# Kernel tuning notes

Measured on AMD Instinct MI355X. Metric: run time of the kernel, lower is better.

## Reference

```python
import jax, jax.numpy as jnp
import numpy as np
from jax.scipy.special import gammaln, xlogy

H, K, V = 8, 64, 192          # heads, key_size, value_size
F = 192                        # num_relative_position_features
LN2 = 0.6931471805599453


def positional_features(T):
    """Enformer positional basis: exp half-life, central mask, gamma pdf;
    non-symmetric -> concat [emb, sign(pos)*emb]. Returns [2T-1, F]."""
    n = F // 6                                  # basis per class per symmetry
    pos = jnp.arange(-(T - 1), T, dtype=jnp.float32)   # [2T-1]
    ap = jnp.abs(pos)[:, None]                  # [2T-1, 1]
    # exponential (min_half_life=3.0, seq_length=T)
    max_range = jnp.log(float(T)) / LN2
    half_life = 2.0 ** jnp.linspace(3.0, max_range, n)
    fe = jnp.exp(-LN2 / half_life * ap)
    # central mask
    widths = 2.0 ** jnp.arange(1, n + 1, dtype=jnp.float32) - 1.0
    fm = (widths > ap).astype(jnp.float32)
    # gamma (stddev=T/(2n), start_mean=T/n)
    stddev = T / (2.0 * n)
    mean = jnp.linspace(T / float(n), float(T), n)
    conc = (mean / stddev) ** 2
    rate = mean / stddev ** 2
    log_p = xlogy(conc - 1.0, ap) - rate * ap - (gammaln(conc) - conc * jnp.log(rate))
    prob = jnp.exp(log_p) + 1e-8
    fg = prob / jnp.max(prob)
    emb = jnp.concatenate([fe, fm, fg], axis=-1)               # [2T-1, F/2]
    emb = jnp.concatenate([emb, jnp.sign(pos)[:, None] * emb], axis=-1)  # [2T-1, F]
    return emb


def relative_shift(x):
    """TransformerXL relative shift. x: [B,H,T,2T-1] -> [B,H,T,T]."""
    b, h, t1, r = x.shape                       # r == 2*t1 - 1
    x = jnp.pad(x, ((0, 0), (0, 0), (0, 0), (1, 0)))  # [B,H,T,2T]
    x = x.reshape(b, h, r + 1, t1)[:, :, 1:, :]        # [B,H,2T-1,T]
    x = x.reshape(b, h, t1, r)
    return x[..., :t1]


def setup_inputs() -> dict:
    key = jax.random.key(0)
    ks = jax.random.split(key, 8)
    B, T, D = 2, 1536, 1536
    s = 0.02
    return {
        "x": jax.random.normal(ks[0], (B, T, D), jnp.float32),
        "Wq": jax.random.normal(ks[1], (D, H * K), jnp.float32) * s,
        "Wk": jax.random.normal(ks[2], (D, H * K), jnp.float32) * s,
        "Wv": jax.random.normal(ks[3], (D, H * V), jnp.float32) * s,
        "Wrk": jax.random.normal(ks[4], (F, H * K), jnp.float32) * s,
        "Wemb": jax.random.normal(ks[5], (H * V, D), jnp.float32) * s,
        "r_w_bias": jax.random.normal(ks[6], (1, H, 1, K), jnp.float32) * s,
        "r_r_bias": jax.random.normal(ks[7], (1, H, 1, K), jnp.float32) * s,
    }


def reference(x, Wq, Wk, Wv, Wrk, Wemb, r_w_bias, r_r_bias):
    B, T, D = x.shape
    q = (x @ Wq).reshape(B, T, H, K).transpose(0, 2, 1, 3)   # [B,H,T,K]
    k = (x @ Wk).reshape(B, T, H, K).transpose(0, 2, 1, 3)
    v = (x @ Wv).reshape(B, T, H, V).transpose(0, 2, 1, 3)   # [B,H,T,V]
    q = q * (K ** -0.5)                                       # scaling
    emb = positional_features(T)                              # [2T-1, F]
    r_k = (emb @ Wrk).reshape(2 * T - 1, H, K).transpose(1, 0, 2)  # [H,2T-1,K]
    content = jnp.einsum('bhqk,bhmk->bhqm', q + r_w_bias, k)       # [B,H,T,T]
    rel = jnp.einsum('bhqk,hmk->bhqm', q + r_r_bias, r_k)          # [B,H,T,2T-1]
    logits = content + relative_shift(rel)
    w = jax.nn.softmax(logits, axis=-1)
    out = jnp.einsum('bhqm,bhmv->bhqv', w, v)                      # [B,H,T,V]
    out = out.transpose(0, 2, 1, 3).reshape(B, T, H * V)
    return out @ Wemb
```

## Files before the change

### kernel.cpp

```cpp
#include <hip/hip_runtime.h>
#include <stdint.h>

#define DEVI __device__ __forceinline__

typedef short bf16x8 __attribute__((ext_vector_type(8)));
typedef float f32x4 __attribute__((ext_vector_type(4)));

#define PMAX 0.01867013f

DEVI float b2f(unsigned short u) {
  union { unsigned u32; float f; } x;
  x.u32 = ((unsigned)u) << 16;
  return x.f;
}
DEVI unsigned short f2b(float f) {
  union { float f32; unsigned u32; } x;
  x.f32 = f;
  unsigned u = x.u32;
  return (unsigned short)((u + 0x7FFFu + ((u >> 16) & 1u)) >> 16);
}

DEVI void gload16(const unsigned short* g, unsigned short* l) {
  __builtin_amdgcn_global_load_lds(
      (const __attribute__((address_space(1))) void*)g,
      (__attribute__((address_space(3))) void*)l, 16, 0, 0);
}

DEVI float gamma_prob(float ap, int i) {
  float mean = 48.f * (float)(i + 1);
  float conc = (mean / 24.f) * (mean / 24.f);
  float rate = mean / 576.f;
  if (ap == 0.f) return 1e-8f;
  float logp = (conc - 1.f) * logf(ap) - rate * ap - (lgammaf(conc) - conc * logf(rate));
  return expf(logp) + 1e-8f;
}

DEVI void dev_transpose(const float* srcf, const unsigned short* srcb, int src_ld,
                        unsigned short* dst, int dst_ld, int rows, int cols,
                        int bx, int by, unsigned short (*t)[33]) {
  int tx = threadIdx.x & 31, ty = threadIdx.x >> 5;
  int r0 = by * 32, c0 = bx * 32;
#pragma unroll
  for (int i = 0; i < 4; i++) {
    int r = r0 + ty + i * 8, cc = c0 + tx;
    if (r < rows && cc < cols)
      t[ty + i * 8][tx] = srcf ? f2b(srcf[(size_t)r * src_ld + cc])
                               : srcb[(size_t)r * src_ld + cc];
  }
  __syncthreads();
#pragma unroll
  for (int i = 0; i < 4; i++) {
    int dr = c0 + ty + i * 8, dc = r0 + tx;
    if (dr < cols && dc < rows) dst[(size_t)dr * dst_ld + dc] = t[tx][ty + i * 8];
  }
}

__global__ __launch_bounds__(256) void k_prep(
    const float* __restrict__ x, const float* __restrict__ Wq,
    const float* __restrict__ Wk, const float* __restrict__ Wv,
    const float* __restrict__ Wemb, const float* __restrict__ Wrk,
    unsigned short* __restrict__ xb, unsigned short* __restrict__ WqkvT,
    unsigned short* __restrict__ WembT, unsigned short* __restrict__ WrkT,
    unsigned short* __restrict__ emb) {
  __shared__ unsigned short t[32][33];
  int bid = blockIdx.x;
  if (bid < 4608) {
    int i = (bid * 256 + threadIdx.x) * 4;
    float4 v = *(const float4*)(x + i);
    ushort4 o;
    o.x = f2b(v.x); o.y = f2b(v.y); o.z = f2b(v.z); o.w = f2b(v.w);
    *(ushort4*)(xb + i) = o;
  } else if (bid < 5376) {
    int s = bid - 4608;
    dev_transpose(Wq, nullptr, 512, WqkvT, 1536, 1536, 512, s % 16, s / 16, t);
  } else if (bid < 6144) {
    int s = bid - 5376;
    dev_transpose(Wk, nullptr, 512, WqkvT + (size_t)512 * 1536, 1536, 1536, 512, s % 16, s / 16, t);
  } else if (bid < 8448) {
    int s = bid - 6144;
    dev_transpose(Wv, nullptr, 1536, WqkvT + (size_t)1024 * 1536, 1536, 1536, 1536, s % 48, s / 48, t);
  } else if (bid < 10752) {
    int s = bid - 8448;
    dev_transpose(Wemb, nullptr, 1536, WembT, 1536, 1536, 1536, s % 48, s / 48, t);
  } else if (bid < 10848) {
    int s = bid - 10752;
    dev_transpose(Wrk, nullptr, 512, WrkT, 192, 192, 512, s % 16, s / 16, t);
  } else {
    int idx = (bid - 10848) * 256 + threadIdx.x;
    if (idx < 3071 * 96) {
      int m = idx / 96, cc = idx % 96;
      float ap = fabsf((float)(m - 1535));
      float val;
      if (cc < 32) {
        float max_range = logf(1536.f) * 1.4426950408889634f;
        float l = 3.f + (float)cc * (max_range - 3.f) / 31.f;
        val = exp2f(-ap * exp2f(-l));
      } else if (cc < 64) {
        float width = exp2f((float)(cc - 31)) - 1.f;
        val = (width > ap) ? 1.f : 0.f;
      } else {
        val = gamma_prob(ap, cc - 64) / PMAX;
      }
      float sgn = (m > 1535) ? 1.f : ((m < 1535) ? -1.f : 0.f);
      emb[(size_t)m * 192 + cc] = f2b(val);
      emb[(size_t)m * 192 + 96 + cc] = f2b(sgn * val);
    }
  }
}

DEVI void dev_gemm(const unsigned short* __restrict__ A, const unsigned short* __restrict__ Bt,
                   unsigned short* Cb, float* Cf, int M, int N, int K,
                   int bx, int by, unsigned short* As, unsigned short* Bs) {
  int tid = threadIdx.x;
  int w = tid >> 6, L = tid & 63, g = L >> 4, c = L & 15;
  int m0 = by << 7, n0 = bx << 7;
  int wm = (w >> 1) << 6, wn = (w & 1) << 6;
  f32x4 acc[4][4];
#pragma unroll
  for (int i = 0; i < 4; i++)
#pragma unroll
    for (int j = 0; j < 4; j++) acc[i][j] = (f32x4){0.f, 0.f, 0.f, 0.f};
  int nkt = K >> 5;
  for (int kt = 0; kt < nkt; kt++) {
    int k0 = kt << 5;
#pragma unroll
    for (int i2 = 0; i2 < 2; i2++) {
      int cidx = tid + (i2 << 8);
      int row = cidx >> 2, kc = (cidx & 3) << 3;
      int ra = m0 + row;
      if (ra >= M) ra = M - 1;
      gload16(A + (size_t)ra * K + k0 + kc, As + cidx * 8);
      gload16(Bt + (size_t)(n0 + row) * K + k0 + kc, Bs + cidx * 8);
    }
    __syncthreads();
    bf16x8 af[4], bfr[4];
#pragma unroll
    for (int t = 0; t < 4; t++) af[t] = *(const bf16x8*)(As + (wm + t * 16 + c) * 32 + g * 8);
#pragma unroll
    for (int t = 0; t < 4; t++) bfr[t] = *(const bf16x8*)(Bs + (wn + t * 16 + c) * 32 + g * 8);
#pragma unroll
    for (int mt = 0; mt < 4; mt++)
#pragma unroll
      for (int nt = 0; nt < 4; nt++)
        acc[mt][nt] = __builtin_amdgcn_mfma_f32_16x16x32_bf16(af[mt], bfr[nt], acc[mt][nt], 0, 0, 0);
    __syncthreads();
  }
#pragma unroll
  for (int mt = 0; mt < 4; mt++)
#pragma unroll
    for (int nt = 0; nt < 4; nt++)
#pragma unroll
      for (int r = 0; r < 4; r++) {
        int rr = m0 + wm + mt * 16 + g * 4 + r;
        if (rr < M) {
          size_t o = (size_t)rr * N + n0 + wn + nt * 16 + c;
          if (Cf) Cf[o] = acc[mt][nt][r];
          else Cb[o] = f2b(acc[mt][nt][r]);
        }
      }
}

__global__ __launch_bounds__(256) void k_gemm(
    const unsigned short* __restrict__ A, const unsigned short* __restrict__ Bt,
    unsigned short* Cb, float* Cf, int M, int N, int K) {
  __shared__ unsigned short sm[8192];
  dev_gemm(A, Bt, Cb, Cf, M, N, K, blockIdx.x, blockIdx.y, sm, sm + 4096);
}

__global__ __launch_bounds__(256) void k_mid(
    const unsigned short* __restrict__ emb, const unsigned short* __restrict__ WrkT,
    unsigned short* __restrict__ rkb, const unsigned short* __restrict__ QKV,
    unsigned short* __restrict__ Vt) {
  __shared__ unsigned short sm[8192];
  int bid = blockIdx.x;
  if (bid < 96) {
    dev_gemm(emb, WrkT, rkb, nullptr, 3071, 512, 192, bid & 3, bid >> 2, sm, sm + 4096);
  } else {
    int tt = bid - 96;
    int which = tt / 2304;
    tt %= 2304;
    dev_transpose(nullptr, QKV + 1024 + (size_t)which * 1536 * 2560, 2560,
                  Vt + (size_t)which * 1536 * 1536, 1536, 1536, 1536,
                  tt % 48, tt / 48, (unsigned short (*)[33])sm);
  }
}

__global__ __launch_bounds__(256, 2) void k_attn(
    const unsigned short* __restrict__ QKV, const unsigned short* __restrict__ rk,
    const unsigned short* __restrict__ Vt, const float* __restrict__ rwb,
    const float* __restrict__ rrb, unsigned short* __restrict__ O) {
  __shared__ float smem[9344];
  const int tid = threadIdx.x;
  const int w = tid >> 6, L = tid & 63, g = L >> 4, c = L & 15;
  const int bid = blockIdx.x;
  const int h = bid & 7, b = (bid >> 3) & 1;
  const int i0b = (bid >> 4) << 5;
  const int bh = b * 8 + h;

  bf16x8 aqw[2][2], aqr[2][2];
#pragma unroll
  for (int qi = 0; qi < 2; qi++) {
    const unsigned short* qrow =
        QKV + (size_t)(b * 1536 + i0b + qi * 16 + c) * 2560 + h * 64;
#pragma unroll
    for (int ks = 0; ks < 2; ks++) {
      union { bf16x8 v; unsigned short s[8]; } uw, ur;
#pragma unroll
      for (int j = 0; j < 8; j++) {
        int d = ks * 32 + g * 8 + j;
        float qv = b2f(qrow[d]) * 0.125f;
        uw.s[j] = f2b(qv + rwb[h * 64 + d]);
        ur.s[j] = f2b(qv + rrb[h * 64 + d]);
      }
      aqw[qi][ks] = uw.v;
      aqr[qi][ks] = ur.v;
    }
  }

  int baddr[4], bsel[4];
#pragma unroll
  for (int r = 0; r < 4; r++) {
    int u = c - (g * 4 + r) + 15;
    baddr[r] = (((g << 4) | (u & 15)) << 2);
    bsel[r] = (u >> 4) & 1;
  }

  f32x4 Ofr[2][12];
#pragma unroll
  for (int qi = 0; qi < 2; qi++)
#pragma unroll
    for (int t = 0; t < 12; t++) Ofr[qi][t] = (f32x4){0.f, 0.f, 0.f, 0.f};
  float lrow[2][4] = {{0.f, 0.f, 0.f, 0.f}, {0.f, 0.f, 0.f, 0.f}};

  const size_t kbase = (size_t)(b * 1536) * 2560 + 512 + h * 64;
  const unsigned short* vtb = Vt + (size_t)(bh * 192) * 1536;
  const unsigned short* rkh = rk + h * 64;

  for (int jt = 0; jt < 6; jt++) {
    const int j0 = w * 384 + jt * 64;
    const int moff1 = j0 - (i0b + 16) + 1520;
    unsigned short* pwbA = (unsigned short*)smem + ((jt & 1) * 8 + w * 2 + 0) * 1152;
    unsigned short* pwbB = (unsigned short*)smem + ((jt & 1) * 8 + w * 2 + 1) * 1152;

    f32x4 Sc[2][4];
#pragma unroll
    for (int nt = 0; nt < 4; nt++) {
      const unsigned short* krow = QKV + kbase + (size_t)(j0 + nt * 16 + c) * 2560;
      bf16x8 kf0 = *(const bf16x8*)(krow + g * 8);
      bf16x8 kf1 = *(const bf16x8*)(krow + 32 + g * 8);
      f32x4 z0 = (f32x4){0.f, 0.f, 0.f, 0.f};
      z0 = __builtin_amdgcn_mfma_f32_16x16x32_bf16(aqw[0][0], kf0, z0, 0, 0, 0);
      z0 = __builtin_amdgcn_mfma_f32_16x16x32_bf16(aqw[0][1], kf1, z0, 0, 0, 0);
      Sc[0][nt] = z0;
      f32x4 z1 = (f32x4){0.f, 0.f, 0.f, 0.f};
      z1 = __builtin_amdgcn_mfma_f32_16x16x32_bf16(aqw[1][0], kf0, z1, 0, 0, 0);
      z1 = __builtin_amdgcn_mfma_f32_16x16x32_bf16(aqw[1][1], kf1, z1, 0, 0, 0);
      Sc[1][nt] = z1;
    }

    float bandp0[4], bandp1[4];
    {
      int mg = moff1 + c;
      const unsigned short* rrow = rkh + (size_t)mg * 512;
      bf16x8 rf0 = *(const bf16x8*)(rrow + g * 8);
      bf16x8 rf1 = *(const bf16x8*)(rrow + 32 + g * 8);
      f32x4 z = (f32x4){0.f, 0.f, 0.f, 0.f};
      z = __builtin_amdgcn_mfma_f32_16x16x32_bf16(aqr[1][0], rf0, z, 0, 0, 0);
      z = __builtin_amdgcn_mfma_f32_16x16x32_bf16(aqr[1][1], rf1, z, 0, 0, 0);
#pragma unroll
      for (int r = 0; r < 4; r++)
        bandp1[r] = __int_as_float(__builtin_amdgcn_ds_bpermute(baddr[r], __float_as_int(z[r])));
    }
#pragma unroll
    for (int j = 1; j <= 5; j++) {
      int mg = moff1 + 16 * j + c;
      if (mg > 3070) mg = 3070;
      const unsigned short* rrow = rkh + (size_t)mg * 512;
      bf16x8 rf0 = *(const bf16x8*)(rrow + g * 8);
      bf16x8 rf1 = *(const bf16x8*)(rrow + 32 + g * 8);
      {
        f32x4 z = (f32x4){0.f, 0.f, 0.f, 0.f};
        z = __builtin_amdgcn_mfma_f32_16x16x32_bf16(aqr[0][0], rf0, z, 0, 0, 0);
        z = __builtin_amdgcn_mfma_f32_16x16x32_bf16(aqr[0][1], rf1, z, 0, 0, 0);
        if (j == 1) {
#pragma unroll
          for (int r = 0; r < 4; r++)
            bandp0[r] = __int_as_float(__builtin_amdgcn_ds_bpermute(baddr[r], __float_as_int(z[r])));
        } else {
          const int nt = j - 2;
#pragma unroll
          for (int r = 0; r < 4; r++) {
            float bandc = __int_as_float(__builtin_amdgcn_ds_bpermute(baddr[r], __float_as_int(z[r])));
            Sc[0][nt][r] += bsel[r] ? bandc : bandp0[r];
            bandp0[r] = bandc;
          }
        }
      }
      if (j <= 4) {
        f32x4 z = (f32x4){0.f, 0.f, 0.f, 0.f};
        z = __builtin_amdgcn_mfma_f32_16x16x32_bf16(aqr[1][0], rf0, z, 0, 0, 0);
        z = __builtin_amdgcn_mfma_f32_16x16x32_bf16(aqr[1][1], rf1, z, 0, 0, 0);
        const int nt = j - 1;
#pragma unroll
        for (int r = 0; r < 4; r++) {
          float bandc = __int_as_float(__builtin_amdgcn_ds_bpermute(baddr[r], __float_as_int(z[r])));
          Sc[1][nt][r] += bsel[r] ? bandc : bandp1[r];
          bandp1[r] = bandc;
        }
      }
    }

#pragma unroll
    for (int nt = 0; nt < 4; nt++)
#pragma unroll
      for (int r = 0; r < 4; r++) {
        float pA = __expf(Sc[0][nt][r]);
        lrow[0][r] += pA;
        pwbA[(g * 4 + r) * 72 + nt * 16 + c] = f2b(pA);
        float pB = __expf(Sc[1][nt][r]);
        lrow[1][r] += pB;
        pwbB[(g * 4 + r) * 72 + nt * 16 + c] = f2b(pB);
      }
    __builtin_amdgcn_sched_barrier(0x7F);
    bf16x8 apA0 = *(const bf16x8*)(pwbA + c * 72 + g * 8);
    bf16x8 apA1 = *(const bf16x8*)(pwbA + c * 72 + 32 + g * 8);
    bf16x8 apB0 = *(const bf16x8*)(pwbB + c * 72 + g * 8);
    bf16x8 apB1 = *(const bf16x8*)(pwbB + c * 72 + 32 + g * 8);
    __builtin_amdgcn_sched_barrier(0x7F);

    __builtin_amdgcn_s_setprio(1);
#pragma unroll
    for (int nt3 = 0; nt3 < 12; nt3++) {
      const unsigned short* vrow = vtb + (size_t)(nt3 * 16 + c) * 1536 + j0;
      bf16x8 v0 = *(const bf16x8*)(vrow + g * 8);
      bf16x8 v1 = *(const bf16x8*)(vrow + 32 + g * 8);
      Ofr[0][nt3] = __builtin_amdgcn_mfma_f32_16x16x32_bf16(apA0, v0, Ofr[0][nt3], 0, 0, 0);
      Ofr[1][nt3] = __builtin_amdgcn_mfma_f32_16x16x32_bf16(apB0, v0, Ofr[1][nt3], 0, 0, 0);
      Ofr[0][nt3] = __builtin_amdgcn_mfma_f32_16x16x32_bf16(apA1, v1, Ofr[0][nt3], 0, 0, 0);
      Ofr[1][nt3] = __builtin_amdgcn_mfma_f32_16x16x32_bf16(apB1, v1, Ofr[1][nt3], 0, 0, 0);
    }
    __builtin_amdgcn_s_setprio(0);
  }

#pragma unroll
  for (int qi = 0; qi < 2; qi++)
#pragma unroll
    for (int r = 0; r < 4; r++) {
      float s = lrow[qi][r];
      s += __shfl_xor(s, 1, 64);
      s += __shfl_xor(s, 2, 64);
      s += __shfl_xor(s, 4, 64);
      s += __shfl_xor(s, 8, 64);
      lrow[qi][r] = s;
    }
  float* mll = smem + 9216;
  if (c == 0)
#pragma unroll
    for (int qi = 0; qi < 2; qi++)
#pragma unroll
      for (int r = 0; r < 4; r++) mll[qi * 64 + w * 16 + g * 4 + r] = lrow[qi][r];
  __syncthreads();
  float scale[2][4];
#pragma unroll
  for (int qi = 0; qi < 2; qi++)
#pragma unroll
    for (int r = 0; r < 4; r++) {
      int q = qi * 64 + g * 4 + r;
      scale[qi][r] = 1.f / (mll[q] + mll[16 + q] + mll[32 + q] + mll[48 + q]);
    }
#pragma unroll
  for (int qi = 0; qi < 2; qi++)
#pragma unroll
    for (int t = 0; t < 12; t++)
#pragma unroll
      for (int r = 0; r < 4; r++) Ofr[qi][t][r] *= scale[qi][r];

  const int qo = tid >> 4, v3 = (tid & 15) * 3;
#pragma unroll
  for (int qi = 0; qi < 2; qi++) {
    unsigned short* orow =
        O + (size_t)(b * 1536 + i0b + qi * 16 + qo) * 1536 + h * 192;
#pragma unroll
    for (int c4 = 0; c4 < 4; c4++) {
      __syncthreads();
      float* slot = smem + w * 768;
#pragma unroll
      for (int tl = 0; tl < 3; tl++)
#pragma unroll
        for (int r = 0; r < 4; r++)
          slot[(g * 4 + r) * 48 + tl * 16 + c] = Ofr[qi][c4 * 3 + tl][r];
      __syncthreads();
#pragma unroll
      for (int k = 0; k < 3; k++) {
        int v = v3 + k;
        float s = smem[qo * 48 + v] + smem[768 + qo * 48 + v] +
                  smem[1536 + qo * 48 + v] + smem[2304 + qo * 48 + v];
        orow[c4 * 48 + v] = f2b(s);
      }
    }
  }
}

extern "C" void kernel_launch(void* const* d_in, const int* in_sizes, int n_in,
                              void* d_out, int out_size, void* d_ws, size_t ws_size,
                              hipStream_t stream) {
  const float* x    = (const float*)d_in[0];
  const float* Wq   = (const float*)d_in[1];
  const float* Wk   = (const float*)d_in[2];
  const float* Wv   = (const float*)d_in[3];
  const float* Wrk  = (const float*)d_in[4];
  const float* Wemb = (const float*)d_in[5];
  const float* rwb  = (const float*)d_in[6];
  const float* rrb  = (const float*)d_in[7];

  char* ws = (char*)d_ws;
  size_t off = 0;
  auto alloc = [&](size_t bytes) -> void* {
    void* p = ws + off;
    off += (bytes + 255) & ~(size_t)255;
    return p;
  };
  unsigned short* xb    = (unsigned short*)alloc((size_t)3072 * 1536 * 2);
  unsigned short* WqkvT = (unsigned short*)alloc((size_t)2560 * 1536 * 2);
  unsigned short* WembT = (unsigned short*)alloc((size_t)1536 * 1536 * 2);
  unsigned short* WrkT  = (unsigned short*)alloc((size_t)512 * 192 * 2);
  unsigned short* QKV   = (unsigned short*)alloc((size_t)3072 * 2560 * 2);
  unsigned short* Vt    = (unsigned short*)alloc((size_t)2 * 1536 * 1536 * 2);
  unsigned short* emb   = (unsigned short*)alloc((size_t)3072 * 192 * 2);
  unsigned short* rkb   = (unsigned short*)alloc((size_t)3072 * 512 * 2);
  unsigned short* Obuf  = (unsigned short*)alloc((size_t)3072 * 1536 * 2);

  k_prep<<<12000, 256, 0, stream>>>(x, Wq, Wk, Wv, Wemb, Wrk, xb, WqkvT, WembT, WrkT, emb);
  k_gemm<<<dim3(20, 24), 256, 0, stream>>>(xb, WqkvT, QKV, nullptr, 3072, 2560, 1536);
  k_mid<<<4704, 256, 0, stream>>>(emb, WrkT, rkb, QKV, Vt);
  k_attn<<<768, 256, 0, stream>>>(QKV, rkb, Vt, rwb, rrb, Obuf);
  k_gemm<<<dim3(12, 24), 256, 0, stream>>>(Obuf, WembT, nullptr, (float*)d_out, 3072, 1536, 1536);
}
```

Before: 313.9 us.

## Restructure attention into 128-query blocks with LDS-staged K/V and split-key partials

Each attention block now covers 128 queries and half of the keys. K and V^T tiles are staged into swizzled LDS through async global-to-LDS loads, with K double-buffered, and the probability tiles of all four waves are shared so each wave computes a 48-wide V slice for all 128 queries. Unnormalized fp32 partial outputs and row sums are written per key half, and a new finalize kernel sums the halves, normalizes and converts to bf16. This raises K/V reuse and cuts redundant global loads, but adds a large fp32 partial buffer round trip, an extra launch, and per-tile block barriers.

Result: faster. 278.0 us (-11.4%).

```diff
diff --git a/kernel.cpp b/kernel.cpp
--- a/kernel.cpp
+++ b/kernel.cpp
@@ -188,20 +188,26 @@
 __global__ __launch_bounds__(256, 2) void k_attn(
     const unsigned short* __restrict__ QKV, const unsigned short* __restrict__ rk,
     const unsigned short* __restrict__ Vt, const float* __restrict__ rwb,
-    const float* __restrict__ rrb, unsigned short* __restrict__ O) {
-  __shared__ float smem[9344];
+    const float* __restrict__ rrb, float* __restrict__ Opart,
+    float* __restrict__ lpart) {
+  __shared__ unsigned short lds[28672];
   const int tid = threadIdx.x;
   const int w = tid >> 6, L = tid & 63, g = L >> 4, c = L & 15;
   const int bid = blockIdx.x;
-  const int h = bid & 7, b = (bid >> 3) & 1;
-  const int i0b = (bid >> 4) << 5;
+  const int h = bid & 7, b = (bid >> 3) & 1, kh = (bid >> 4) & 1;
+  const int i0b = (bid >> 5) << 7;
+  const int qp = i0b + w * 32;
   const int bh = b * 8 + h;
+  const int c7s = (c & 7) << 3;
+
+  const int lrow8 = L >> 3;
+  const int lbo = (((L & 7) * 16) ^ ((lrow8 & 7) << 4));
 
   bf16x8 aqw[2][2], aqr[2][2];
 #pragma unroll
   for (int qi = 0; qi < 2; qi++) {
     const unsigned short* qrow =
-        QKV + (size_t)(b * 1536 + i0b + qi * 16 + c) * 2560 + h * 64;
+        QKV + (size_t)(b * 1536 + qp + qi * 16 + c) * 2560 + h * 64;
 #pragma unroll
     for (int ks = 0; ks < 2; ks++) {
       union { bf16x8 v; unsigned short s[8]; } uw, ur;
@@ -225,29 +231,54 @@
     bsel[r] = (u >> 4) & 1;
   }
 
-  f32x4 Ofr[2][12];
-#pragma unroll
-  for (int qi = 0; qi < 2; qi++)
-#pragma unroll
-    for (int t = 0; t < 12; t++) Ofr[qi][t] = (f32x4){0.f, 0.f, 0.f, 0.f};
+  f32x4 Ofr[8][3];
+#pragma unroll
+  for (int s = 0; s < 8; s++)
+#pragma unroll
+    for (int t = 0; t < 3; t++) Ofr[s][t] = (f32x4){0.f, 0.f, 0.f, 0.f};
   float lrow[2][4] = {{0.f, 0.f, 0.f, 0.f}, {0.f, 0.f, 0.f, 0.f}};
 
-  const size_t kbase = (size_t)(b * 1536) * 2560 + 512 + h * 64;
-  const unsigned short* vtb = Vt + (size_t)(bh * 192) * 1536;
   const unsigned short* rkh = rk + h * 64;
-
-  for (int jt = 0; jt < 6; jt++) {
-    const int j0 = w * 384 + jt * 64;
-    const int moff1 = j0 - (i0b + 16) + 1520;
-    unsigned short* pwbA = (unsigned short*)smem + ((jt & 1) * 8 + w * 2 + 0) * 1152;
-    unsigned short* pwbB = (unsigned short*)smem + ((jt & 1) * 8 + w * 2 + 1) * 1152;
+  const size_t kgbase = (size_t)(b * 1536 + kh * 768) * 2560 + 512 + h * 64;
+  const size_t vgbase = (size_t)(bh * 192) * 1536 + kh * 768;
+
+  auto stageK = [&](int kt, int nb) {
+#pragma unroll
+    for (int i = 0; i < 2; i++) {
+      int key = w * 16 + i * 8 + lrow8;
+      const unsigned short* src =
+          QKV + kgbase + (size_t)(kt * 64 + key) * 2560 + (lbo >> 1);
+      gload16(src, lds + nb * 4096 + w * 1024 + i * 512);
+    }
+  };
+  auto stageV = [&](int kt) {
+#pragma unroll
+    for (int i = 0; i < 6; i++) {
+      int vd = w * 48 + i * 8 + lrow8;
+      const unsigned short* src =
+          Vt + vgbase + (size_t)vd * 1536 + kt * 64 + (lbo >> 1);
+      gload16(src, lds + 8192 + w * 3072 + i * 512);
+    }
+  };
+
+  stageK(0, 0);
+  __syncthreads();
+
+  for (int jt = 0; jt < 12; jt++) {
+    const int cur = jt & 1;
+    stageV(jt);
+    if (jt < 11) stageK(jt + 1, cur ^ 1);
+
+    const int j0g = kh * 768 + jt * 64;
+    const int moff1 = j0g - (qp + 16) + 1520;
+    const unsigned short* kb = lds + cur * 4096;
 
     f32x4 Sc[2][4];
 #pragma unroll
     for (int nt = 0; nt < 4; nt++) {
-      const unsigned short* krow = QKV + kbase + (size_t)(j0 + nt * 16 + c) * 2560;
-      bf16x8 kf0 = *(const bf16x8*)(krow + g * 8);
-      bf16x8 kf1 = *(const bf16x8*)(krow + 32 + g * 8);
+      const int kro = (nt * 16 + c) * 64;
+      bf16x8 kf0 = *(const bf16x8*)(kb + kro + ((g * 8) ^ c7s));
+      bf16x8 kf1 = *(const bf16x8*)(kb + kro + ((32 + g * 8) ^ c7s));
       f32x4 z0 = (f32x4){0.f, 0.f, 0.f, 0.f};
       z0 = __builtin_amdgcn_mfma_f32_16x16x32_bf16(aqw[0][0], kf0, z0, 0, 0, 0);
       z0 = __builtin_amdgcn_mfma_f32_16x16x32_bf16(aqw[0][1], kf1, z0, 0, 0, 0);
@@ -262,11 +293,9 @@
     {
       int mg = moff1 + c;
       const unsigned short* rrow = rkh + (size_t)mg * 512;
-      bf16x8 rf0 = *(const bf16x8*)(rrow + g * 8);
-      bf16x8 rf1 = *(const bf16x8*)(rrow + 32 + g * 8);
       f32x4 z = (f32x4){0.f, 0.f, 0.f, 0.f};
-      z = __builtin_amdgcn_mfma_f32_16x16x32_bf16(aqr[1][0], rf0, z, 0, 0, 0);
-      z = __builtin_amdgcn_mfma_f32_16x16x32_bf16(aqr[1][1], rf1, z, 0, 0, 0);
+      z = __builtin_amdgcn_mfma_f32_16x16x32_bf16(aqr[1][0], *(const bf16x8*)(rrow + g * 8), z, 0, 0, 0);
+      z = __builtin_amdgcn_mfma_f32_16x16x32_bf16(aqr[1][1], *(const bf16x8*)(rrow + 32 + g * 8), z, 0, 0, 0);
 #pragma unroll
       for (int r = 0; r < 4; r++)
         bandp1[r] = __int_as_float(__builtin_amdgcn_ds_bpermute(baddr[r], __float_as_int(z[r])));
@@ -311,35 +340,43 @@
     }
 
 #pragma unroll
-    for (int nt = 0; nt < 4; nt++)
-#pragma unroll
-      for (int r = 0; r < 4; r++) {
-        float pA = __expf(Sc[0][nt][r]);
-        lrow[0][r] += pA;
-        pwbA[(g * 4 + r) * 72 + nt * 16 + c] = f2b(pA);
-        float pB = __expf(Sc[1][nt][r]);
-        lrow[1][r] += pB;
-        pwbB[(g * 4 + r) * 72 + nt * 16 + c] = f2b(pB);
-      }
-    __builtin_amdgcn_sched_barrier(0x7F);
-    bf16x8 apA0 = *(const bf16x8*)(pwbA + c * 72 + g * 8);
-    bf16x8 apA1 = *(const bf16x8*)(pwbA + c * 72 + 32 + g * 8);
-    bf16x8 apB0 = *(const bf16x8*)(pwbB + c * 72 + g * 8);
-    bf16x8 apB1 = *(const bf16x8*)(pwbB + c * 72 + 32 + g * 8);
-    __builtin_amdgcn_sched_barrier(0x7F);
-
+    for (int qi = 0; qi < 2; qi++) {
+      unsigned short* slab = lds + 20480 + (2 * w + qi) * 1024;
+#pragma unroll
+      for (int nt = 0; nt < 4; nt++)
+#pragma unroll
+        for (int r = 0; r < 4; r++) {
+          float p = __expf(Sc[qi][nt][r]);
+          lrow[qi][r] += p;
+          int q = g * 4 + r;
+          slab[q * 64 + ((nt * 16 + c) ^ ((q & 7) << 3))] = f2b(p);
+        }
+    }
+
+    __syncthreads();
+
+    bf16x8 vf0[3], vf1[3];
+#pragma unroll
+    for (int vt = 0; vt < 3; vt++) {
+      const int vro = 8192 + (w * 48 + vt * 16 + c) * 64;
+      vf0[vt] = *(const bf16x8*)(lds + vro + ((g * 8) ^ c7s));
+      vf1[vt] = *(const bf16x8*)(lds + vro + ((32 + g * 8) ^ c7s));
+    }
     __builtin_amdgcn_s_setprio(1);
 #pragma unroll
-    for (int nt3 = 0; nt3 < 12; nt3++) {
-      const unsigned short* vrow = vtb + (size_t)(nt3 * 16 + c) * 1536 + j0;
-      bf16x8 v0 = *(const bf16x8*)(vrow + g * 8);
-      bf16x8 v1 = *(const bf16x8*)(vrow + 32 + g * 8);
-      Ofr[0][nt3] = __builtin_amdgcn_mfma_f32_16x16x32_bf16(apA0, v0, Ofr[0][nt3], 0, 0, 0);
-      Ofr[1][nt3] = __builtin_amdgcn_mfma_f32_16x16x32_bf16(apB0, v0, Ofr[1][nt3], 0, 0, 0);
-      Ofr[0][nt3] = __builtin_amdgcn_mfma_f32_16x16x32_bf16(apA1, v1, Ofr[0][nt3], 0, 0, 0);
-      Ofr[1][nt3] = __builtin_amdgcn_mfma_f32_16x16x32_bf16(apB1, v1, Ofr[1][nt3], 0, 0, 0);
+    for (int s = 0; s < 8; s++) {
+      const unsigned short* slab = lds + 20480 + s * 1024;
+      bf16x8 ap0 = *(const bf16x8*)(slab + c * 64 + ((g * 8) ^ c7s));
+      bf16x8 ap1 = *(const bf16x8*)(slab + c * 64 + ((32 + g * 8) ^ c7s));
+#pragma unroll
+      for (int vt = 0; vt < 3; vt++) {
+        Ofr[s][vt] = __builtin_amdgcn_mfma_f32_16x16x32_bf16(ap0, vf0[vt], Ofr[s][vt], 0, 0, 0);
+        Ofr[s][vt] = __builtin_amdgcn_mfma_f32_16x16x32_bf16(ap1, vf1[vt], Ofr[s][vt], 0, 0, 0);
+      }
     }
     __builtin_amdgcn_s_setprio(0);
+
+    __syncthreads();
   }
 
 #pragma unroll
@@ -353,51 +390,46 @@
       s += __shfl_xor(s, 8, 64);
       lrow[qi][r] = s;
     }
-  float* mll = smem + 9216;
-  if (c == 0)
+  if (c == 0) {
 #pragma unroll
     for (int qi = 0; qi < 2; qi++)
 #pragma unroll
-      for (int r = 0; r < 4; r++) mll[qi * 64 + w * 16 + g * 4 + r] = lrow[qi][r];
-  __syncthreads();
-  float scale[2][4];
-#pragma unroll
-  for (int qi = 0; qi < 2; qi++)
-#pragma unroll
-    for (int r = 0; r < 4; r++) {
-      int q = qi * 64 + g * 4 + r;
-      scale[qi][r] = 1.f / (mll[q] + mll[16 + q] + mll[32 + q] + mll[48 + q]);
-    }
-#pragma unroll
-  for (int qi = 0; qi < 2; qi++)
-#pragma unroll
-    for (int t = 0; t < 12; t++)
-#pragma unroll
-      for (int r = 0; r < 4; r++) Ofr[qi][t][r] *= scale[qi][r];
-
-  const int qo = tid >> 4, v3 = (tid & 15) * 3;
-#pragma unroll
-  for (int qi = 0; qi < 2; qi++) {
-    unsigned short* orow =
-        O + (size_t)(b * 1536 + i0b + qi * 16 + qo) * 1536 + h * 192;
-#pragma unroll
-    for (int c4 = 0; c4 < 4; c4++) {
-      __syncthreads();
-      float* slot = smem + w * 768;
-#pragma unroll
-      for (int tl = 0; tl < 3; tl++)
-#pragma unroll
-        for (int r = 0; r < 4; r++)
-          slot[(g * 4 + r) * 48 + tl * 16 + c] = Ofr[qi][c4 * 3 + tl][r];
-      __syncthreads();
-#pragma unroll
-      for (int k = 0; k < 3; k++) {
-        int v = v3 + k;
-        float s = smem[qo * 48 + v] + smem[768 + qo * 48 + v] +
-                  smem[1536 + qo * 48 + v] + smem[2304 + qo * 48 + v];
-        orow[c4 * 48 + v] = f2b(s);
-      }
-    }
+      for (int r = 0; r < 4; r++)
+        lpart[(size_t)((kh * 2 + b) * 8 + h) * 1536 + qp + qi * 16 + g * 4 + r] =
+            lrow[qi][r];
+  }
+#pragma unroll
+  for (int s = 0; s < 8; s++)
+#pragma unroll
+    for (int vt = 0; vt < 3; vt++)
+#pragma unroll
+      for (int r = 0; r < 4; r++)
+        Opart[(size_t)(kh * 3072 + b * 1536 + i0b + s * 16 + g * 4 + r) * 1536 +
+              h * 192 + w * 48 + vt * 16 + c] = Ofr[s][vt][r];
+}
+
+__global__ __launch_bounds__(256) void k_fin(
+    const float* __restrict__ Op, const float* __restrict__ lp,
+    unsigned short* __restrict__ O) {
+  int idx = (blockIdx.x * 256 + threadIdx.x) * 8;
+  int row = idx / 1536, c0 = idx % 1536;
+  int b = row >> 11 ? 1 : (row >= 1536);
+  b = row >= 1536;
+  int q = row - b * 1536, hh = c0 / 192;
+  float l = lp[(size_t)(b * 8 + hh) * 1536 + q] +
+            lp[(size_t)((2 + b) * 8 + hh) * 1536 + q];
+  float sc = 1.f / l;
+  const float4* p0 = (const float4*)(Op + (size_t)row * 1536 + c0);
+  const float4* p1 = (const float4*)(Op + (size_t)(3072 + row) * 1536 + c0);
+#pragma unroll
+  for (int half = 0; half < 2; half++) {
+    float4 a = p0[half], bb = p1[half];
+    ushort4 o;
+    o.x = f2b((a.x + bb.x) * sc);
+    o.y = f2b((a.y + bb.y) * sc);
+    o.z = f2b((a.z + bb.z) * sc);
+    o.w = f2b((a.w + bb.w) * sc);
+    *(ushort4*)(O + (size_t)row * 1536 + c0 + half * 4) = o;
   }
 }
 
@@ -429,10 +461,13 @@
   unsigned short* emb   = (unsigned short*)alloc((size_t)3072 * 192 * 2);
   unsigned short* rkb   = (unsigned short*)alloc((size_t)3072 * 512 * 2);
   unsigned short* Obuf  = (unsigned short*)alloc((size_t)3072 * 1536 * 2);
+  float*          Opart = (float*)alloc((size_t)2 * 3072 * 1536 * 4);
+  float*          lpart = (float*)alloc((size_t)2 * 2 * 8 * 1536 * 4);
 
   k_prep<<<12000, 256, 0, stream>>>(x, Wq, Wk, Wv, Wemb, Wrk, xb, WqkvT, WembT, WrkT, emb);
   k_gemm<<<dim3(20, 24), 256, 0, stream>>>(xb, WqkvT, QKV, nullptr, 3072, 2560, 1536);
   k_mid<<<4704, 256, 0, stream>>>(emb, WrkT, rkb, QKV, Vt);
-  k_attn<<<768, 256, 0, stream>>>(QKV, rkb, Vt, rwb, rrb, Obuf);
+  k_attn<<<384, 256, 0, stream>>>(QKV, rkb, Vt, rwb, rrb, Opart, lpart);
+  k_fin<<<2304, 256, 0, stream>>>(Opart, lpart, Obuf);
   k_gemm<<<dim3(12, 24), 256, 0, stream>>>(Obuf, WembT, nullptr, (float*)d_out, 3072, 1536, 1536);
 }
```
